# Kernel optimization log

Measured on AMD Instinct MI355X. Metric: run time of the kernel, lower is better.

Reference implementation:

```python
import jax, jax.numpy as jnp
import numpy as np

N_NODES = 100000
NUM_FEAT = 64
NUM_CLASS = 40
N_EDGES = 1600000


def setup_inputs() -> dict:
    key = jax.random.key(0)
    k1, k2, k3, k4, k5 = jax.random.split(key, 5)
    x = jax.random.normal(k1, (N_NODES, NUM_FEAT), dtype=jnp.float32)
    index = jax.random.randint(k2, (2, N_EDGES), 0, N_NODES, dtype=jnp.int64)
    # SAGEConv params: lin_l applied to aggregated neighbors (has bias),
    # lin_r applied to root features (no bias) -- PyG convention.
    s = 1.0 / np.sqrt(NUM_FEAT)
    lin_l_w = jax.random.uniform(k3, (NUM_FEAT, NUM_CLASS), dtype=jnp.float32, minval=-s, maxval=s)
    lin_l_b = jnp.zeros((NUM_CLASS,), dtype=jnp.float32)
    lin_r_w = jax.random.uniform(k4, (NUM_FEAT, NUM_CLASS), dtype=jnp.float32, minval=-s, maxval=s)
    return {"x": x, "index": index, "lin_l_w": lin_l_w, "lin_l_b": lin_l_b, "lin_r_w": lin_r_w}


def reference(x, index, lin_l_w, lin_l_b, lin_r_w):
    src, dst = index[0], index[1]
    # Mean aggregation over incoming neighbors: messages flow src -> dst.
    msg = x[src]                                        # [E, F] gather
    agg_sum = jax.ops.segment_sum(msg, dst, num_segments=N_NODES)   # [N, F]
    deg = jax.ops.segment_sum(jnp.ones((index.shape[1],), dtype=x.dtype), dst,
                              num_segments=N_NODES)     # [N]
    agg = agg_sum / jnp.maximum(deg, 1.0)[:, None]      # mean, safe for isolated nodes
    out = agg @ lin_l_w + lin_l_b + x @ lin_r_w         # [N, C]
    return jax.nn.log_softmax(out, axis=1)
```

## Files before the change

kernel.cpp:

```cpp
#include <hip/hip_runtime.h>
#include <hip/hip_fp8.h>
#include <math.h>

constexpr int NODES = 100000;
constexpr int F = 64;
constexpr int C = 40;
constexpr int NPB   = 128;
constexpr int NB    = (NODES + NPB - 1) / NPB;
constexpr int NBPAD = 1024;
constexpr int BCAP  = 2816;
constexpr int TILE  = 4096;
constexpr int NTILES = NODES / 16;
constexpr int MBLK  = (NTILES + 3) / 4;

typedef __attribute__((ext_vector_type(8))) short short8;
typedef __attribute__((ext_vector_type(4))) float floatx4;
typedef __attribute__((ext_vector_type(2))) float floatx2;

__device__ inline unsigned bf16pack2(float a, float b) {
    unsigned ua = __builtin_bit_cast(unsigned, a);
    unsigned ub = __builtin_bit_cast(unsigned, b);
    ua += 0x7FFFu + ((ua >> 16) & 1u);
    ub += 0x7FFFu + ((ub >> 16) & 1u);
    return (ua >> 16) | (ub & 0xFFFF0000u);
}
__device__ inline unsigned short bf16of(float a) {
    unsigned ua = __builtin_bit_cast(unsigned, a);
    ua += 0x7FFFu + ((ua >> 16) & 1u);
    return (unsigned short)(ua >> 16);
}
__device__ inline float bf16tof(unsigned short u) {
    return __builtin_bit_cast(float, (unsigned)u << 16);
}
__device__ inline unsigned char fp8of(float f) {
    __hip_fp8_e4m3 q(f);
    return (unsigned char)q.__x;
}
template <int K>
__device__ inline float fp8byte(unsigned d) {
    __hip_fp8_e4m3 v;
    v.__x = (__hip_fp8_storage_t)((d >> (8 * K)) & 0xFFu);
    return (float)v;
}
template <int HI>
__device__ inline floatx2 fp8pk(unsigned d) {
#if __has_builtin(__builtin_amdgcn_cvt_pk_f32_fp8)
    return __builtin_amdgcn_cvt_pk_f32_fp8((int)d, HI != 0);
#else
    floatx2 r;
    r[0] = fp8byte<HI ? 2 : 0>(d);
    r[1] = fp8byte<HI ? 3 : 1>(d);
    return r;
#endif
}

__global__ __launch_bounds__(256)
void fused_A(const float* __restrict__ x,
             const float* __restrict__ wl,
             const float* __restrict__ bl,
             const float* __restrict__ wr,
             const int* __restrict__ src, const int* __restrict__ dst,
             int* __restrict__ gcursor, int* __restrict__ bbuf, int nedges,
             unsigned char* __restrict__ y8f, unsigned short* __restrict__ z8) {
    __shared__ union {
        struct { int lhist[NB]; int lcur[NB]; } bz;
        struct { unsigned sB[10 * 64 * 4]; float sbl[40]; } mf;
    } sh;

    int t = threadIdx.x;

    if (blockIdx.x < MBLK) {
        if (t < 40) sh.mf.sbl[t] = bl[t];
        for (int s = t; s < 640; s += 256) {
            int region = s >> 6;
            int l      = s & 63;
            int ct = region >> 1, ks = region & 1;
            int col = ct * 16 + (l & 15);
            int fb  = ks * 32 + ((l >> 4) << 3);
            const float* wsrc = (col < 40) ? (wl + col) : (wr + (col - 40));
            unsigned* dstp = &sh.mf.sB[s * 4];
#pragma unroll
            for (int p = 0; p < 4; ++p) {
                float a = wsrc[(fb + 2 * p) * 40];
                float b = wsrc[(fb + 2 * p + 1) * 40];
                dstp[p] = bf16pack2(a, b);
            }
        }
        __syncthreads();

        int lane = t & 63;
        int nt = blockIdx.x * 4 + (t >> 6);
        if (nt >= NTILES) return;

        union U { unsigned u[4]; short8 v; };
        short8 bf[5][2];
#pragma unroll
        for (int ct = 0; ct < 5; ++ct)
#pragma unroll
            for (int ks = 0; ks < 2; ++ks) {
                U tmp;
                const uint4* p =
                    (const uint4*)&sh.mf.sB[((ct * 2 + ks) * 64 + lane) * 4];
                uint4 q = *p;
                tmp.u[0] = q.x; tmp.u[1] = q.y; tmp.u[2] = q.z; tmp.u[3] = q.w;
                bf[ct][ks] = tmp.v;
            }

        floatx4 acc[5];
#pragma unroll
        for (int ct = 0; ct < 5; ++ct) {
            int col = ct * 16 + (lane & 15);
            float bias = (col >= 40) ? sh.mf.sbl[col - 40] : 0.0f;
            acc[ct] = (floatx4){bias, bias, bias, bias};
        }

        int row = nt * 16 + (lane & 15);
        const float4* xp = (const float4*)(x + (size_t)row * F);
        short8 af[2];
#pragma unroll
        for (int ks = 0; ks < 2; ++ks) {
            int kb = ks * 8 + ((lane >> 4) << 1);
            float4 va = xp[kb];
            float4 vb = xp[kb + 1];
            U a;
            a.u[0] = bf16pack2(va.x, va.y);
            a.u[1] = bf16pack2(va.z, va.w);
            a.u[2] = bf16pack2(vb.x, vb.y);
            a.u[3] = bf16pack2(vb.z, vb.w);
            af[ks] = a.v;
        }

#pragma unroll
        for (int ks = 0; ks < 2; ++ks)
#pragma unroll
            for (int ct = 0; ct < 5; ++ct)
                acc[ct] = __builtin_amdgcn_mfma_f32_16x16x32_bf16(
                    af[ks], bf[ct][ks], acc[ct], 0, 0, 0);

#pragma unroll
        for (int ct = 0; ct < 5; ++ct) {
            int col = ct * 16 + (lane & 15);
#pragma unroll
            for (int r = 0; r < 4; ++r) {
                int grow = nt * 16 + ((lane >> 4) << 2) + r;
                if (col < 40) y8f[(size_t)grow * C + col]       = fp8of(acc[ct][r]);
                else          z8[(size_t)grow * C + (col - 40)] = bf16of(acc[ct][r]);
            }
        }
    } else {
        for (int i = t; i < NB; i += 256) sh.bz.lhist[i] = 0;
        __syncthreads();

        int bb = blockIdx.x - MBLK;
        int base = bb * TILE;
        int pk[16], bk[16];
#pragma unroll
        for (int u = 0; u < 16; ++u) {
            int e = base + u * 256 + t;
            bk[u] = -1;
            if (e < nedges) {
                int s = src[e], d = dst[e];
                if ((unsigned)s < (unsigned)NODES && (unsigned)d < (unsigned)NODES) {
                    bk[u] = d >> 7;
                    pk[u] = s | ((d & 127) << 17);
                    atomicAdd(&sh.bz.lhist[bk[u]], 1);
                }
            }
        }
        __syncthreads();
        for (int i = t; i < NB; i += 256) {
            int c = sh.bz.lhist[i];
            sh.bz.lcur[i] = c ? atomicAdd(&gcursor[i], c) : 0;
        }
        __syncthreads();
#pragma unroll
        for (int u = 0; u < 16; ++u) {
            if (bk[u] >= 0) {
                int p = atomicAdd(&sh.bz.lcur[bk[u]], 1);
                if (p < BCAP) bbuf[(size_t)bk[u] * BCAP + p] = pk[u];
            }
        }
    }
}

__device__ inline void acc8(float (&acc)[8], uint2 q) {
    floatx2 v;
    v = fp8pk<0>(q.x); acc[0] += v[0]; acc[1] += v[1];
    v = fp8pk<1>(q.x); acc[2] += v[0]; acc[3] += v[1];
    v = fp8pk<0>(q.y); acc[4] += v[0]; acc[5] += v[1];
    v = fp8pk<1>(q.y); acc[6] += v[0]; acc[7] += v[1];
}

__global__ __launch_bounds__(256)
void sort_aggregate(const unsigned char* __restrict__ y8f,
                    const unsigned short* __restrict__ z8,
                    const int* __restrict__ bbuf,
                    const int* __restrict__ gcount,
                    float* __restrict__ out) {
    __shared__ int lhist[NPB];
    __shared__ int lcur[NPB];
    __shared__ int slds[BCAP];
    __shared__ int w0tot;

    int b = blockIdx.x;
    int t = threadIdx.x;
    int lane = t & 63;

    if (t < NPB) lhist[t] = 0;
    __syncthreads();

    int cnt = gcount[b];
    if (cnt > BCAP) cnt = BCAP;
    const int* myb = bbuf + (size_t)b * BCAP;

    for (int i = t; i < cnt; i += 256)
        atomicAdd(&lhist[myb[i] >> 17], 1);
    __syncthreads();

    int c = 0, sc = 0;
    if (t < NPB) {
        c = lhist[t];
        sc = c;
#pragma unroll
        for (int d = 1; d < 64; d <<= 1) {
            int o = __shfl_up(sc, d);
            if (lane >= d) sc += o;
        }
    }
    if (t == 63) w0tot = sc;
    __syncthreads();
    if (t >= 64 && t < NPB) sc += w0tot;
    if (t < NPB) lcur[t] = sc - c;
    __syncthreads();

    for (int i = t; i < cnt; i += 256) {
        int pk = myb[i];
        int p = atomicAdd(&lcur[pk >> 17], 1);
        slds[p] = pk & 0x1FFFF;
    }
    __syncthreads();

    int gid = t >> 3;
    int i = t & 7;
    bool valid = (i < 5);
    int byteoff = (valid ? i : 4) * 8;

    for (int j = 0; j < 4; ++j) {
        int nd = gid * 4 + j;
        int n = b * NPB + nd;
        if (n >= NODES) break;

        int dg = lhist[nd];
        const int* sp = slds + (lcur[nd] - dg);

        uint4 zv = make_uint4(0u, 0u, 0u, 0u);
        if (valid) zv = *(const uint4*)(z8 + (size_t)n * C + i * 8);

        float acc[8] = {0.f, 0.f, 0.f, 0.f, 0.f, 0.f, 0.f, 0.f};

        int npair = dg >> 1;
        if (npair > 0) {
            int s0 = sp[0];
            int s1 = sp[1];
            for (int p = 0; p < npair; ++p) {
                int c0 = s0, c1 = s1;
                int nx = 2 * p + 2;
                int pi = (nx + 1 < dg) ? nx : dg - 2;
                s0 = sp[pi];
                s1 = sp[pi + 1];
                uint2 q0 = *(const uint2*)(y8f + (size_t)c0 * C + byteoff);
                uint2 q1 = *(const uint2*)(y8f + (size_t)c1 * C + byteoff);
                acc8(acc, q0);
                acc8(acc, q1);
            }
        }
        if (dg & 1) {
            int cl = sp[dg - 1];
            uint2 q = *(const uint2*)(y8f + (size_t)cl * C + byteoff);
            acc8(acc, q);
        }

        float inv = 1.0f / (float)(dg > 0 ? dg : 1);

        float o[8];
        if (valid) {
            unsigned zu[4] = {zv.x, zv.y, zv.z, zv.w};
#pragma unroll
            for (int k = 0; k < 4; ++k) {
                o[2 * k]     = bf16tof((unsigned short)(zu[k] & 0xFFFFu))
                             + acc[2 * k] * inv;
                o[2 * k + 1] = bf16tof((unsigned short)(zu[k] >> 16))
                             + acc[2 * k + 1] * inv;
            }
        } else {
#pragma unroll
            for (int k = 0; k < 8; ++k) o[k] = -1e30f;
        }

        float mv = -1e30f;
        if (valid)
#pragma unroll
            for (int k = 0; k < 8; ++k) mv = fmaxf(mv, o[k]);
#pragma unroll
        for (int m = 1; m <= 4; m <<= 1) mv = fmaxf(mv, __shfl_xor(mv, m));

        float ev = 0.0f;
        if (valid)
#pragma unroll
            for (int k = 0; k < 8; ++k) ev += __expf(o[k] - mv);
#pragma unroll
        for (int m = 1; m <= 4; m <<= 1) ev += __shfl_xor(ev, m);
        float lse = mv + __logf(ev);

        if (valid) {
            float4 o0 = make_float4(o[0] - lse, o[1] - lse, o[2] - lse, o[3] - lse);
            float4 o1 = make_float4(o[4] - lse, o[5] - lse, o[6] - lse, o[7] - lse);
            float4* op = (float4*)(out + (size_t)n * C + i * 8);
            op[0] = o0;
            op[1] = o1;
        }
    }
}

__global__ __launch_bounds__(256)
void scatter_kernel(const float* __restrict__ x, const int* __restrict__ src,
                    const int* __restrict__ dst, float* __restrict__ aggsum,
                    float* __restrict__ deg, int nedges) {
    int lane = threadIdx.x & 63;
    int e = blockIdx.x * 4 + (threadIdx.x >> 6);
    if (e >= nedges) return;
    int s = src[e], d = dst[e];
    if ((unsigned)s >= (unsigned)NODES || (unsigned)d >= (unsigned)NODES) return;
    atomicAdd(&aggsum[(size_t)d * F + lane], x[(size_t)s * F + lane]);
    if (lane == 0) atomicAdd(&deg[d], 1.0f);
}

__global__ __launch_bounds__(256)
void meanify_kernel(float* __restrict__ aggsum, const float* __restrict__ deg) {
    int lane = threadIdx.x & 63;
    int n = blockIdx.x * 4 + (threadIdx.x >> 6);
    if (n >= NODES) return;
    aggsum[(size_t)n * F + lane] *= 1.0f / fmaxf(deg[n], 1.0f);
}

__global__ __launch_bounds__(256)
void node_kernel(const float* __restrict__ x, const float* __restrict__ aggmean,
                 const float* __restrict__ wl, const float* __restrict__ bl,
                 const float* __restrict__ wr, float* __restrict__ out) {
    __shared__ alignas(16) float sWl[F * C];
    __shared__ alignas(16) float sWr[F * C];
    __shared__ alignas(16) float sb[C];
    for (int i = threadIdx.x; i < F * C; i += 256) { sWl[i] = wl[i]; sWr[i] = wr[i]; }
    if (threadIdx.x < C) sb[threadIdx.x] = bl[threadIdx.x];
    __syncthreads();
    int n = blockIdx.x * 256 + threadIdx.x;
    if (n >= NODES) return;
    float4 acc[10];
    const float4* sb4 = (const float4*)sb;
#pragma unroll
    for (int q = 0; q < 10; ++q) acc[q] = sb4[q];
    const float4* xr  = (const float4*)(x       + (size_t)n * F);
    const float4* ar  = (const float4*)(aggmean + (size_t)n * F);
    const float4* wl4 = (const float4*)sWl;
    const float4* wr4 = (const float4*)sWr;
    for (int f4 = 0; f4 < F / 4; ++f4) {
        float4 xv = xr[f4], av = ar[f4];
        float xs[4]  = {xv.x, xv.y, xv.z, xv.w};
        float as_[4] = {av.x, av.y, av.z, av.w};
#pragma unroll
        for (int jj = 0; jj < 4; ++jj) {
            int f = f4 * 4 + jj;
#pragma unroll
            for (int q = 0; q < 10; ++q) {
                float4 wlv = wl4[f * 10 + q], wrv = wr4[f * 10 + q];
                acc[q].x = fmaf(as_[jj], wlv.x, fmaf(xs[jj], wrv.x, acc[q].x));
                acc[q].y = fmaf(as_[jj], wlv.y, fmaf(xs[jj], wrv.y, acc[q].y));
                acc[q].z = fmaf(as_[jj], wlv.z, fmaf(xs[jj], wrv.z, acc[q].z));
                acc[q].w = fmaf(as_[jj], wlv.w, fmaf(xs[jj], wrv.w, acc[q].w));
            }
        }
    }
    float m = -1e30f;
#pragma unroll
    for (int q = 0; q < 10; ++q)
        m = fmaxf(m, fmaxf(fmaxf(acc[q].x, acc[q].y), fmaxf(acc[q].z, acc[q].w)));
    float ssum = 0.0f;
#pragma unroll
    for (int q = 0; q < 10; ++q)
        ssum += __expf(acc[q].x - m) + __expf(acc[q].y - m) +
                __expf(acc[q].z - m) + __expf(acc[q].w - m);
    float lse = m + __logf(ssum);
    float4* op = (float4*)(out + (size_t)n * C);
#pragma unroll
    for (int q = 0; q < 10; ++q) {
        float4 v;
        v.x = acc[q].x - lse; v.y = acc[q].y - lse;
        v.z = acc[q].z - lse; v.w = acc[q].w - lse;
        op[q] = v;
    }
}

extern "C" void kernel_launch(void* const* d_in, const int* in_sizes, int n_in,
                              void* d_out, int out_size, void* d_ws, size_t ws_size,
                              hipStream_t stream) {
    const float* x     = (const float*)d_in[0];
    const int*   index = (const int*)d_in[1];
    const float* wl    = (const float*)d_in[2];
    const float* bl    = (const float*)d_in[3];
    const float* wr    = (const float*)d_in[4];
    float* out = (float*)d_out;

    int nedges = in_sizes[1] / 2;
    const int* src = index;
    const int* dst = index + nedges;

    size_t need = (size_t)NODES * C * 3
                + ((size_t)NB * BCAP + NBPAD) * 4;

    if (ws_size >= need) {
        unsigned short* z8 = (unsigned short*)d_ws;
        unsigned char* y8f = (unsigned char*)(z8 + (size_t)NODES * C);
        int* bbuf       = (int*)(y8f + (size_t)NODES * C);
        int* gcursor    = bbuf + (size_t)NB * BCAP;

        hipMemsetAsync(gcursor, 0, NBPAD * sizeof(int), stream);

        int bblocks = (nedges + TILE - 1) / TILE;
        fused_A<<<MBLK + bblocks, 256, 0, stream>>>(
            x, wl, bl, wr, src, dst, gcursor, bbuf, nedges, y8f, z8);
        sort_aggregate<<<NB, 256, 0, stream>>>(
            y8f, z8, bbuf, gcursor, out);
    } else {
        float* aggsum = (float*)d_ws;
        float* deg    = aggsum + (size_t)NODES * F;
        hipMemsetAsync(d_ws, 0,
                       ((size_t)NODES * F + NODES) * sizeof(float), stream);
        scatter_kernel<<<(nedges + 3) / 4, 256, 0, stream>>>(
            x, src, dst, aggsum, deg, nedges);
        meanify_kernel<<<(NODES + 3) / 4, 256, 0, stream>>>(aggsum, deg);
        node_kernel<<<(NODES + 255) / 256, 256, 0, stream>>>(
            x, aggsum, wl, bl, wr, out);
    }
}
```

Measured before the change: 139.8 us.

## Pad fp8 neighbor rows to 64 bytes, unroll gather by four, nontemporal output stores

Pads the fp8 projected neighbor table to a 64-byte row pitch so each gathered row sits inside one cache line instead of straddling two. Bucket entries are loaded once into registers and reused for both the histogram and scatter passes rather than read from global memory twice. The neighbor gather loop now keeps four loads in flight instead of two. Output stores use nontemporal hints. The padding raises workspace use and write footprint, and the extra registers for the entry cache and the wider unroll may lower occupancy.

```diff
diff --git a/kernel.cpp b/kernel.cpp
--- a/kernel.cpp
+++ b/kernel.cpp
@@ -5,10 +5,12 @@
 constexpr int NODES = 100000;
 constexpr int F = 64;
 constexpr int C = 40;
+constexpr int YPITCH = 64;
 constexpr int NPB   = 128;
 constexpr int NB    = (NODES + NPB - 1) / NPB;
 constexpr int NBPAD = 1024;
 constexpr int BCAP  = 2816;
+constexpr int EK    = (BCAP + 255) / 256;
 constexpr int TILE  = 4096;
 constexpr int NTILES = NODES / 16;
 constexpr int MBLK  = (NTILES + 3) / 4;
@@ -16,6 +18,8 @@
 typedef __attribute__((ext_vector_type(8))) short short8;
 typedef __attribute__((ext_vector_type(4))) float floatx4;
 typedef __attribute__((ext_vector_type(2))) float floatx2;
+typedef __attribute__((ext_vector_type(4))) unsigned uintx4;
+typedef __attribute__((ext_vector_type(4))) float fx4;
 
 __device__ inline unsigned bf16pack2(float a, float b) {
     unsigned ua = __builtin_bit_cast(unsigned, a);
@@ -143,7 +147,7 @@
 #pragma unroll
             for (int r = 0; r < 4; ++r) {
                 int grow = nt * 16 + ((lane >> 4) << 2) + r;
-                if (col < 40) y8f[(size_t)grow * C + col]       = fp8of(acc[ct][r]);
+                if (col < 40) y8f[(size_t)grow * YPITCH + col] = fp8of(acc[ct][r]);
                 else          z8[(size_t)grow * C + (col - 40)] = bf16of(acc[ct][r]);
             }
         }
@@ -213,8 +217,16 @@
     if (cnt > BCAP) cnt = BCAP;
     const int* myb = bbuf + (size_t)b * BCAP;
 
-    for (int i = t; i < cnt; i += 256)
-        atomicAdd(&lhist[myb[i] >> 17], 1);
+    int ek[EK];
+#pragma unroll
+    for (int u = 0; u < EK; ++u) {
+        int i = t + u * 256;
+        ek[u] = (i < cnt) ? myb[i] : -1;
+    }
+#pragma unroll
+    for (int u = 0; u < EK; ++u) {
+        if (ek[u] >= 0) atomicAdd(&lhist[ek[u] >> 17], 1);
+    }
     __syncthreads();
 
     int c = 0, sc = 0;
@@ -233,10 +245,13 @@
     if (t < NPB) lcur[t] = sc - c;
     __syncthreads();
 
-    for (int i = t; i < cnt; i += 256) {
-        int pk = myb[i];
-        int p = atomicAdd(&lcur[pk >> 17], 1);
-        slds[p] = pk & 0x1FFFF;
+#pragma unroll
+    for (int u = 0; u < EK; ++u) {
+        int pk = ek[u];
+        if (pk >= 0) {
+            int p = atomicAdd(&lcur[pk >> 17], 1);
+            slds[p] = pk & 0x1FFFF;
+        }
     }
     __syncthreads();
 
@@ -253,30 +268,35 @@
         int dg = lhist[nd];
         const int* sp = slds + (lcur[nd] - dg);
 
-        uint4 zv = make_uint4(0u, 0u, 0u, 0u);
-        if (valid) zv = *(const uint4*)(z8 + (size_t)n * C + i * 8);
+        uintx4 zv = {0u, 0u, 0u, 0u};
+        if (valid) zv = *(const uintx4*)(z8 + (size_t)n * C + i * 8);
 
         float acc[8] = {0.f, 0.f, 0.f, 0.f, 0.f, 0.f, 0.f, 0.f};
 
-        int npair = dg >> 1;
-        if (npair > 0) {
-            int s0 = sp[0];
-            int s1 = sp[1];
-            for (int p = 0; p < npair; ++p) {
-                int c0 = s0, c1 = s1;
-                int nx = 2 * p + 2;
-                int pi = (nx + 1 < dg) ? nx : dg - 2;
+        int nquad = dg >> 2;
+        if (nquad > 0) {
+            int s0 = sp[0], s1 = sp[1], s2 = sp[2], s3 = sp[3];
+            for (int p = 0; p < nquad; ++p) {
+                int c0 = s0, c1 = s1, c2 = s2, c3 = s3;
+                int nx = 4 * p + 4;
+                int pi = (nx + 3 < dg) ? nx : dg - 4;
                 s0 = sp[pi];
                 s1 = sp[pi + 1];
-                uint2 q0 = *(const uint2*)(y8f + (size_t)c0 * C + byteoff);
-                uint2 q1 = *(const uint2*)(y8f + (size_t)c1 * C + byteoff);
+                s2 = sp[pi + 2];
+                s3 = sp[pi + 3];
+                uint2 q0 = *(const uint2*)(y8f + (size_t)c0 * YPITCH + byteoff);
+                uint2 q1 = *(const uint2*)(y8f + (size_t)c1 * YPITCH + byteoff);
+                uint2 q2 = *(const uint2*)(y8f + (size_t)c2 * YPITCH + byteoff);
+                uint2 q3 = *(const uint2*)(y8f + (size_t)c3 * YPITCH + byteoff);
                 acc8(acc, q0);
                 acc8(acc, q1);
-            }
-        }
-        if (dg & 1) {
-            int cl = sp[dg - 1];
-            uint2 q = *(const uint2*)(y8f + (size_t)cl * C + byteoff);
+                acc8(acc, q2);
+                acc8(acc, q3);
+            }
+        }
+        for (int e = nquad * 4; e < dg; ++e) {
+            int cl = sp[e];
+            uint2 q = *(const uint2*)(y8f + (size_t)cl * YPITCH + byteoff);
             acc8(acc, q);
         }
 
@@ -284,7 +304,7 @@
 
         float o[8];
         if (valid) {
-            unsigned zu[4] = {zv.x, zv.y, zv.z, zv.w};
+            unsigned zu[4] = {zv[0], zv[1], zv[2], zv[3]};
 #pragma unroll
             for (int k = 0; k < 4; ++k) {
                 o[2 * k]     = bf16tof((unsigned short)(zu[k] & 0xFFFFu))
@@ -313,11 +333,11 @@
         float lse = mv + __logf(ev);
 
         if (valid) {
-            float4 o0 = make_float4(o[0] - lse, o[1] - lse, o[2] - lse, o[3] - lse);
-            float4 o1 = make_float4(o[4] - lse, o[5] - lse, o[6] - lse, o[7] - lse);
-            float4* op = (float4*)(out + (size_t)n * C + i * 8);
-            op[0] = o0;
-            op[1] = o1;
+            fx4 o0 = {o[0] - lse, o[1] - lse, o[2] - lse, o[3] - lse};
+            fx4 o1 = {o[4] - lse, o[5] - lse, o[6] - lse, o[7] - lse};
+            fx4* op = (fx4*)(out + (size_t)n * C + i * 8);
+            __builtin_nontemporal_store(o0, op);
+            __builtin_nontemporal_store(o1, op + 1);
         }
     }
 }
@@ -414,13 +434,13 @@
     const int* src = index;
     const int* dst = index + nedges;
 
-    size_t need = (size_t)NODES * C * 3
+    size_t need = (size_t)NODES * C * 2 + (size_t)NODES * YPITCH
                 + ((size_t)NB * BCAP + NBPAD) * 4;
 
     if (ws_size >= need) {
         unsigned short* z8 = (unsigned short*)d_ws;
         unsigned char* y8f = (unsigned char*)(z8 + (size_t)NODES * C);
-        int* bbuf       = (int*)(y8f + (size_t)NODES * C);
+        int* bbuf       = (int*)(y8f + (size_t)NODES * YPITCH);
         int* gcursor    = bbuf + (size_t)NB * BCAP;
 
         hipMemsetAsync(gcursor, 0, NBPAD * sizeof(int), stream);
```

After: 142.9 us. 2.2% more time.
